# Kernel optimization log

Hardware: AMD Instinct MI355X
Metric: run time of the kernel (lower is better)

## Reference

```python
import jax, jax.numpy as jnp
import numpy as np

N, D, E, OUT = 10000, 15, 320, 30
H_INOUT = 5  # n_heads for in/out attention layers


def mha(q, k, v, wqkv, bqkv, wo, bo, nheads):
    # q,k,v: [B, L, E]; torch.nn.MultiheadAttention math (unbatched per node)
    B, L, Ed = q.shape
    hd = Ed // nheads
    wq, wk, wv = jnp.split(wqkv, 3, axis=0)
    bq, bk, bv = jnp.split(bqkv, 3)
    q2 = (q @ wq.T + bq).reshape(B, L, nheads, hd)
    k2 = (k @ wk.T + bk).reshape(B, -1, nheads, hd)
    v2 = (v @ wv.T + bv).reshape(B, -1, nheads, hd)
    scores = jnp.einsum('blhd,bmhd->bhlm', q2, k2) * (hd ** -0.5)
    a = jax.nn.softmax(scores, axis=-1)
    o = jnp.einsum('bhlm,bmhd->blhd', a, v2).reshape(B, L, Ed)
    return o @ wo.T + bo


def attn_layer(seq, Wq, Wk, Wv, wqkv, bqkv, wo, bo, nheads):
    # AttentionLayer: custom Q/K/V projections then MultiheadAttention
    return mha(seq @ Wq, seq @ Wk, seq @ Wv, wqkv, bqkv, wo, bo, nheads)


def setup_inputs() -> dict:
    key = jax.random.key(0)
    ks = jax.random.split(key, 24)
    s = 0.05  # scale params small for numerically stable softmax
    inp = {
        'X': jax.random.normal(ks[0], (N, E), jnp.float32),
        'in_idx': jax.random.randint(ks[1], (N, D), 0, N),
        'out_idx': jax.random.randint(ks[2], (N, D), 0, N),
        'in_Wq': jax.random.uniform(ks[3], (E, E)) * s,
        'in_Wk': jax.random.uniform(ks[4], (E, E)) * s,
        'in_Wv': jax.random.uniform(ks[5], (E, E)) * s,
        'in_qkv_w': jax.random.normal(ks[6], (3 * E, E)) * s,
        'in_qkv_b': jax.random.normal(ks[7], (3 * E,)) * s,
        'in_o_w': jax.random.normal(ks[8], (E, E)) * s,
        'in_o_b': jax.random.normal(ks[9], (E,)) * s,
        'out_Wq': jax.random.uniform(ks[10], (E, E)) * s,
        'out_Wk': jax.random.uniform(ks[11], (E, E)) * s,
        'out_Wv': jax.random.uniform(ks[12], (E, E)) * s,
        'out_qkv_w': jax.random.normal(ks[13], (3 * E, E)) * s,
        'out_qkv_b': jax.random.normal(ks[14], (3 * E,)) * s,
        'out_o_w': jax.random.normal(ks[15], (E, E)) * s,
        'out_o_b': jax.random.normal(ks[16], (E,)) * s,
        'fin_qkv_w': jax.random.normal(ks[17], (3 * E, E)) * s,
        'fin_qkv_b': jax.random.normal(ks[18], (3 * E,)) * s,
        'fin_o_w': jax.random.normal(ks[19], (E, E)) * s,
        'fin_o_b': jax.random.normal(ks[20], (E,)) * s,
        'W': jax.random.uniform(ks[21], (E, OUT)) * s,
    }
    return inp


def reference(X, in_idx, out_idx, in_Wq, in_Wk, in_Wv, in_qkv_w, in_qkv_b,
              in_o_w, in_o_b, out_Wq, out_Wk, out_Wv, out_qkv_w, out_qkv_b,
              out_o_w, out_o_b, fin_qkv_w, fin_qkv_b, fin_o_w, fin_o_b, W):
    # per-node sequence: [self ; neighbors] -> [N, D+1, E]
    seq_in = jnp.concatenate([X[:, None, :], X[in_idx]], axis=1)
    seq_out = jnp.concatenate([X[:, None, :], X[out_idx]], axis=1)
    a_in = attn_layer(seq_in, in_Wq, in_Wk, in_Wv, in_qkv_w, in_qkv_b,
                      in_o_w, in_o_b, H_INOUT)
    a_out = attn_layer(seq_out, out_Wq, out_Wk, out_Wv, out_qkv_w, out_qkv_b,
                       out_o_w, out_o_b, H_INOUT)
    att = jnp.concatenate([a_in, a_out], axis=1)  # [N, 2(D+1), E]
    fin = mha(att, att, att, fin_qkv_w, fin_qkv_b, fin_o_w, fin_o_b, 1)
    # first token of final attention per node -> project -> ELU
    return jax.nn.elu(fin[:, 0, :] @ W)
```

## Files before the change

kernel.cpp:

```cpp
#include <hip/hip_runtime.h>
#include <hip/hip_bf16.h>

typedef __hip_bfloat16 bf16;
typedef __bf16 nbf;
typedef nbf bf16x8 __attribute__((ext_vector_type(8)));
typedef float f32x4 __attribute__((ext_vector_type(4)));

#define NNODE 10000
#define DDEG  15
#define EE    320
#define LL    16
#define NH    5
#define HD    64
#define OUTD  30
#define PCOLS 1920
#define KF    642
#define TSTB  648

__global__ void detect_dtype_kernel(const unsigned int* __restrict__ X, int* __restrict__ flag)
{
    __shared__ int cnt;
    if (threadIdx.x == 0) cnt = 0;
    __syncthreads();
    int local = 0;
    for (int i = threadIdx.x; i < 1024; i += 256) {
        unsigned int lo = X[i] & 0xFFFFu;
        int e = (int)((lo >> 7) & 0xFFu);
        if (e >= 100 && e <= 140) local++;
    }
    atomicAdd(&cnt, local);
    __syncthreads();
    if (threadIdx.x == 0) *flag = (cnt > 512) ? 1 : 0;
}

__global__ void convert_bf_kernel(const void* __restrict__ src, nbf* __restrict__ dst,
                                  int n, const int* __restrict__ flag)
{
    int i = blockIdx.x * 256 + threadIdx.x;
    if (i >= n) return;
    if (*flag) dst[i] = ((const nbf*)src)[i];
    else       dst[i] = (nbf)(((const float*)src)[i]);
}

#define NSEG 18
struct ConvTab {
    const void* src[NSEG];
    void*       dst[NSEG];
    int         n[NSEG];
    int         tobf[NSEG];
};

__global__ void convert_batch_kernel(ConvTab t, const int* __restrict__ flag)
{
    const int seg = blockIdx.y;
    const int i = blockIdx.x * 256 + threadIdx.x;
    if (i >= t.n[seg]) return;
    float v = (*flag) ? (float)(((const nbf*)t.src[seg])[i]) : ((const float*)t.src[seg])[i];
    if (t.tobf[seg]) ((nbf*)t.dst[seg])[i] = (nbf)v;
    else             ((float*)t.dst[seg])[i] = v;
}

__global__ __launch_bounds__(256) void transpose3_kernel(const void* s0, const void* s1,
        const void* s2, nbf* __restrict__ dstbase, const int* __restrict__ flag)
{
    const void* src = (blockIdx.z == 0) ? s0 : (blockIdx.z == 1) ? s1 : s2;
    nbf* dst = dstbase + (size_t)blockIdx.z * EE * EE;
    __shared__ nbf tile[32][33];
    const int bx = blockIdx.x * 32, by = blockIdx.y * 32;
    const int tx = threadIdx.x & 31, ty = threadIdx.x >> 5;
    const int f = *flag;
    #pragma unroll
    for (int i = 0; i < 4; ++i) {
        const int r = by + ty + i * 8;
        float v = f ? (float)(((const nbf*)src)[(long)r * EE + bx + tx])
                    : ((const float*)src)[(long)r * EE + bx + tx];
        tile[ty + i * 8][tx] = (nbf)v;
    }
    __syncthreads();
    #pragma unroll
    for (int i = 0; i < 4; ++i) {
        const int r = bx + ty + i * 8;
        dst[(long)r * EE + by + tx] = tile[tx][ty + i * 8];
    }
}

__device__ __forceinline__ void stor(float* p, float v) { *p = v; }
__device__ __forceinline__ void stor(bf16* p, float v) { *p = __float2bfloat16(v); }

template<bool AT, bool BT, typename OT>
__global__ __launch_bounds__(256) void gemm_k(const float* __restrict__ A, int lda,
                       const float* __restrict__ B, int ldb,
                       const float* __restrict__ bias,
                       OT* __restrict__ C, int ldc, int M, int Nn, int K)
{
    __shared__ float As[16][65];
    __shared__ float Bs[16][65];
    const int tid = threadIdx.x;
    const int tx = tid & 15, ty = tid >> 4;
    const int n0 = blockIdx.x * 64, m0 = blockIdx.y * 64;
    float acc[4][4] = {};
    for (int k0 = 0; k0 < K; k0 += 16) {
        if constexpr (AT) {
            for (int i = tid; i < 1024; i += 256) {
                int kk = i >> 6, r = i & 63;
                int gm = m0 + r, gk = k0 + kk;
                As[kk][r] = (gm < M && gk < K) ? A[(long)gk * lda + gm] : 0.f;
            }
        } else {
            for (int i = tid; i < 1024; i += 256) {
                int r = i >> 4, kk = i & 15;
                int gm = m0 + r, gk = k0 + kk;
                As[kk][r] = (gm < M && gk < K) ? A[(long)gm * lda + gk] : 0.f;
            }
        }
        if constexpr (BT) {
            for (int i = tid; i < 1024; i += 256) {
                int r = i >> 4, kk = i & 15;
                int gn = n0 + r, gk = k0 + kk;
                Bs[kk][r] = (gn < Nn && gk < K) ? B[(long)gn * ldb + gk] : 0.f;
            }
        } else {
            for (int i = tid; i < 1024; i += 256) {
                int kk = i >> 6, c = i & 63;
                int gk = k0 + kk, gn = n0 + c;
                Bs[kk][c] = (gk < K && gn < Nn) ? B[(long)gk * ldb + gn] : 0.f;
            }
        }
        __syncthreads();
        #pragma unroll
        for (int kk = 0; kk < 16; ++kk) {
            float ra[4], rb[4];
            #pragma unroll
            for (int a = 0; a < 4; ++a) ra[a] = As[kk][ty * 4 + a];
            #pragma unroll
            for (int b = 0; b < 4; ++b) rb[b] = Bs[kk][tx * 4 + b];
            #pragma unroll
            for (int a = 0; a < 4; ++a)
                #pragma unroll
                for (int b = 0; b < 4; ++b)
                    acc[a][b] += ra[a] * rb[b];
        }
        __syncthreads();
    }
    #pragma unroll
    for (int a = 0; a < 4; ++a) {
        int gm = m0 + ty * 4 + a;
        if (gm >= M) continue;
        #pragma unroll
        for (int b = 0; b < 4; ++b) {
            int gn = n0 + tx * 4 + b;
            if (gn >= Nn) continue;
            float v = acc[a][b] + (bias ? bias[gn] : 0.f);
            stor(&C[(long)gm * ldc + gn], v);
        }
    }
}

template<typename OT>
__global__ __launch_bounds__(256) void gemm_mfma(const nbf* __restrict__ A, int lda,
        const nbf* __restrict__ Bt, int ldb, const float* __restrict__ bias,
        OT* __restrict__ C, int ldc, int M, int Nn, int K)
{
    __shared__ __align__(16) nbf As[128][40];
    __shared__ __align__(16) nbf Bs[128][40];
    const int tid = threadIdx.x;
    const int lane = tid & 63, wave = tid >> 6;
    const int wr = (wave >> 1) * 64, wc = (wave & 1) * 64;
    const int m0 = blockIdx.y * 128, n0 = blockIdx.x * 128;
    const int lr = lane & 15, lq = lane >> 4;
    f32x4 acc[4][4];
    #pragma unroll
    for (int i = 0; i < 4; ++i)
        #pragma unroll
        for (int j = 0; j < 4; ++j) { acc[i][j][0]=0.f; acc[i][j][1]=0.f; acc[i][j][2]=0.f; acc[i][j][3]=0.f; }

    for (int k0 = 0; k0 < K; k0 += 32) {
        #pragma unroll
        for (int v = tid; v < 512; v += 256) {
            const int row = v >> 2, cv = (v & 3) << 3;
            const int gk = k0 + cv;
            {
                const int gm = m0 + row;
                bf16x8 val;
                if (gm < M && gk + 8 <= K) {
                    val = *(const bf16x8*)(A + (long)gm * lda + gk);
                } else {
                    union { bf16x8 v8; nbf e[8]; } u;
                    #pragma unroll
                    for (int j = 0; j < 8; ++j) {
                        float x = (gm < M && gk + j < K) ? (float)A[(long)gm * lda + gk + j] : 0.f;
                        u.e[j] = (nbf)x;
                    }
                    val = u.v8;
                }
                *(bf16x8*)&As[row][cv] = val;
            }
            {
                const int gn = n0 + row;
                bf16x8 val;
                if (gn < Nn && gk + 8 <= K) {
                    val = *(const bf16x8*)(Bt + (long)gn * ldb + gk);
                } else {
                    union { bf16x8 v8; nbf e[8]; } u;
                    #pragma unroll
                    for (int j = 0; j < 8; ++j) {
                        float x = (gn < Nn && gk + j < K) ? (float)Bt[(long)gn * ldb + gk + j] : 0.f;
                        u.e[j] = (nbf)x;
                    }
                    val = u.v8;
                }
                *(bf16x8*)&Bs[row][cv] = val;
            }
        }
        __syncthreads();
        bf16x8 af[4], bfv[4];
        #pragma unroll
        for (int i = 0; i < 4; ++i) af[i] = *(const bf16x8*)&As[wr + i * 16 + lr][lq * 8];
        #pragma unroll
        for (int j = 0; j < 4; ++j) bfv[j] = *(const bf16x8*)&Bs[wc + j * 16 + lr][lq * 8];
        #pragma unroll
        for (int i = 0; i < 4; ++i)
            #pragma unroll
            for (int j = 0; j < 4; ++j)
                acc[i][j] = __builtin_amdgcn_mfma_f32_16x16x32_bf16(af[i], bfv[j], acc[i][j], 0, 0, 0);
        __syncthreads();
    }
    #pragma unroll
    for (int i = 0; i < 4; ++i) {
        #pragma unroll
        for (int j = 0; j < 4; ++j) {
            const int gn = n0 + wc + j * 16 + lr;
            if (gn >= Nn) continue;
            const float bv = bias ? bias[gn] : 0.f;
            #pragma unroll
            for (int r = 0; r < 4; ++r) {
                const int gm = m0 + wr + i * 16 + lq * 4 + r;
                if (gm < M) stor(&C[(long)gm * ldc + gn], acc[i][j][r] + bv);
            }
        }
    }
}

#define NJOB 11
struct JobTab {
    const nbf* A[NJOB];
    const nbf* B[NJOB];
    nbf*       C[NJOB];
};

__global__ __launch_bounds__(256) void gemm_mfma_jobs(JobTab jt)
{
    const nbf* A  = jt.A[blockIdx.z];
    const nbf* Bt = jt.B[blockIdx.z];
    nbf* C        = jt.C[blockIdx.z];
    __shared__ __align__(16) nbf As[128][40];
    __shared__ __align__(16) nbf Bs[128][40];
    const int tid = threadIdx.x;
    const int lane = tid & 63, wave = tid >> 6;
    const int wr = (wave >> 1) * 64, wc = (wave & 1) * 64;
    const int m0 = blockIdx.y * 128, n0 = blockIdx.x * 128;
    const int lr = lane & 15, lq = lane >> 4;
    f32x4 acc[4][4];
    #pragma unroll
    for (int i = 0; i < 4; ++i)
        #pragma unroll
        for (int j = 0; j < 4; ++j) { acc[i][j][0]=0.f; acc[i][j][1]=0.f; acc[i][j][2]=0.f; acc[i][j][3]=0.f; }
    for (int k0 = 0; k0 < EE; k0 += 32) {
        #pragma unroll
        for (int v = tid; v < 512; v += 256) {
            const int row = v >> 2, cv = (v & 3) << 3;
            const int gk = k0 + cv;
            const int gm = m0 + row, gn = n0 + row;
            bf16x8 va = {}, vb = {};
            if (gm < EE) va = *(const bf16x8*)(A + (long)gm * EE + gk);
            if (gn < EE) vb = *(const bf16x8*)(Bt + (long)gn * EE + gk);
            *(bf16x8*)&As[row][cv] = va;
            *(bf16x8*)&Bs[row][cv] = vb;
        }
        __syncthreads();
        bf16x8 af[4], bfv[4];
        #pragma unroll
        for (int i = 0; i < 4; ++i) af[i] = *(const bf16x8*)&As[wr + i * 16 + lr][lq * 8];
        #pragma unroll
        for (int j = 0; j < 4; ++j) bfv[j] = *(const bf16x8*)&Bs[wc + j * 16 + lr][lq * 8];
        #pragma unroll
        for (int i = 0; i < 4; ++i)
            #pragma unroll
            for (int j = 0; j < 4; ++j)
                acc[i][j] = __builtin_amdgcn_mfma_f32_16x16x32_bf16(af[i], bfv[j], acc[i][j], 0, 0, 0);
        __syncthreads();
    }
    #pragma unroll
    for (int i = 0; i < 4; ++i)
        #pragma unroll
        for (int j = 0; j < 4; ++j) {
            const int gn = n0 + wc + j * 16 + lr;
            if (gn >= EE) continue;
            #pragma unroll
            for (int r = 0; r < 4; ++r) {
                const int gm = m0 + wr + i * 16 + lq * 4 + r;
                if (gm < EE) C[(long)gm * EE + gn] = (nbf)acc[i][j][r];
            }
        }
}

__global__ __launch_bounds__(320) void compose_bias_kernel(
        const float* __restrict__ in_o_b, const float* __restrict__ out_o_b,
        const float* __restrict__ fin_qkv_w, const float* __restrict__ fin_qkv_b,
        float* __restrict__ bqc_in, nbf* __restrict__ Kcat, nbf* __restrict__ VcatN)
{
    const int which = blockIdx.x;
    const int b = threadIdx.x;
    const float* ob = (which == 2 || which == 4) ? out_o_b : in_o_b;
    const int off = (which == 0) ? 0 : (which <= 2) ? 320 : 640;
    float acc = fin_qkv_b[off + b];
    const float* wr = fin_qkv_w + (long)(off + b) * EE;
    for (int e = 0; e < EE; ++e) acc += ob[e] * wr[e];
    if (which == 0)      bqc_in[b] = acc;
    else if (which == 1) Kcat[(long)640 * EE + b] = (nbf)acc;
    else if (which == 2) Kcat[(long)641 * EE + b] = (nbf)acc;
    else if (which == 3) VcatN[(long)640 * EE + b] = (nbf)acc;
    else                 VcatN[(long)641 * EE + b] = (nbf)acc;
}

__global__ void compose_bfin(const float* __restrict__ fin_o_b, const float* __restrict__ W,
                             float* __restrict__ bfin)
{
    int j = threadIdx.x;
    if (j >= OUTD) return;
    float acc = 0.f;
    for (int e = 0; e < EE; ++e) acc += fin_o_b[e] * W[e * OUTD + j];
    bfin[j] = acc;
}

__global__ void compose_bT(const float* __restrict__ bqc, const nbf* __restrict__ Kcat,
                           float* __restrict__ bT)
{
    int c = blockIdx.x * 256 + threadIdx.x;
    if (c >= KF) return;
    const nbf* kr = Kcat + (long)c * EE;
    float acc = 0.f;
    for (int b = 0; b < EE; ++b) acc += bqc[b] * (float)kr[b];
    bT[c] = acc;
}

__global__ void ut_prep_kernel(const float* __restrict__ WWT, nbf* __restrict__ Ut)
{
    int v = blockIdx.x * 256 + threadIdx.x;
    if (v >= 64 * EE) return;
    int n = v / EE, e = v % EE;
    float val = 0.f;
    if (n < OUTD) val = WWT[(long)n * KF + e];
    else if (n >= 32 && n < 32 + OUTD) val = WWT[(long)(n - 32) * KF + 320 + e];
    Ut[v] = (nbf)val;
}

__global__ __launch_bounds__(256) void row0_kernel(const nbf* __restrict__ P,
        const int* __restrict__ in_idx, nbf* __restrict__ Orow0)
{
    const int tid = threadIdx.x, lane = tid & 63, wave = tid >> 6;
    const int node = blockIdx.x * 4 + wave;
    __shared__ float a_sh[4][16];
    __shared__ int srcs_sh[4][16];
    const int m = lane & 15, q4 = lane >> 4;
    const int src = (m == 0) ? node : in_idx[node * DDEG + m - 1];
    if (q4 == 0) srcs_sh[wave][m] = src;
    const nbf* qrow = P + (long)node * PCOLS;
    const nbf* krow = P + (long)src * PCOLS + 320;
    #pragma unroll
    for (int h = 0; h < NH; ++h) {
        float s = 0.f;
        bf16x8 q1 = *(const bf16x8*)(qrow + h * 64 + q4 * 16);
        bf16x8 q2 = *(const bf16x8*)(qrow + h * 64 + q4 * 16 + 8);
        bf16x8 k1 = *(const bf16x8*)(krow + h * 64 + q4 * 16);
        bf16x8 k2 = *(const bf16x8*)(krow + h * 64 + q4 * 16 + 8);
        #pragma unroll
        for (int j = 0; j < 8; ++j)
            s += (float)q1[j] * (float)k1[j] + (float)q2[j] * (float)k2[j];
        s += __shfl_xor(s, 16);
        s += __shfl_xor(s, 32);
        s *= 0.125f;
        float mxv = s;
        #pragma unroll
        for (int msk = 8; msk >= 1; msk >>= 1) mxv = fmaxf(mxv, __shfl_xor(mxv, msk));
        float e = __expf(s - mxv);
        float es = e;
        #pragma unroll
        for (int msk = 8; msk >= 1; msk >>= 1) es += __shfl_xor(es, msk);
        if (q4 == 0) a_sh[wave][m] = e / es;
        float o = 0.f;
        #pragma unroll
        for (int mm = 0; mm < 16; ++mm)
            o += a_sh[wave][mm] * (float)P[(long)srcs_sh[wave][mm] * PCOLS + 640 + h * 64 + lane];
        Orow0[(long)node * EE + h * 64 + lane] = (nbf)o;
    }
}

__global__ __launch_bounds__(320) void attn_y_kernel(const nbf* __restrict__ P,
        const int* __restrict__ in_idx, const int* __restrict__ out_idx,
        const nbf* __restrict__ Tb, const nbf* __restrict__ Ut,
        float* __restrict__ Ygl, int node_base)
{
    const int bx = blockIdx.x;
    const int lnode = bx >> 1, d = bx & 1;
    const int node = node_base + lnode;
    const int tid = threadIdx.x;
    const int lane = tid & 63, wave = tid >> 6;
    __shared__ __align__(16) nbf v_s[16][328];
    __shared__ __align__(16) nbf p_s[NH][16][16];
    __shared__ float Yp[NH][16][32];
    const int* idx = d ? out_idx : in_idx;
    const long coloff = (long)d * 960;
    const int lr = lane & 15, lq = lane >> 4;
    #pragma unroll
    for (int v = tid; v < 640; v += 320) {
        const int row = v / 40, c8 = (v % 40) * 8;
        const int src = (row == 0) ? node : idx[node * DDEG + row - 1];
        *(bf16x8*)&v_s[row][c8] = *(const bf16x8*)(P + (long)src * PCOLS + coloff + 640 + c8);
    }
    const int msrc = (lr == 0) ? node : idx[node * DDEG + lr - 1];
    const nbf* prow = P + (long)msrc * PCOLS + coloff;
    f32x4 sc = {0.f, 0.f, 0.f, 0.f};
    #pragma unroll
    for (int c = 0; c < 2; ++c) {
        bf16x8 aq = *(const bf16x8*)(prow + wave * 64 + c * 32 + lq * 8);
        bf16x8 bk = *(const bf16x8*)(prow + 320 + wave * 64 + c * 32 + lq * 8);
        sc = __builtin_amdgcn_mfma_f32_16x16x32_bf16(aq, bk, sc, 0, 0, 0);
    }
    float pr[4], mx4[4], sm4[4];
    #pragma unroll
    for (int r = 0; r < 4; ++r) { pr[r] = sc[r] * 0.125f; mx4[r] = pr[r]; }
    #pragma unroll
    for (int msk = 8; msk >= 1; msk >>= 1)
        #pragma unroll
        for (int r = 0; r < 4; ++r) mx4[r] = fmaxf(mx4[r], __shfl_xor(mx4[r], msk));
    #pragma unroll
    for (int r = 0; r < 4; ++r) { pr[r] = __expf(pr[r] - mx4[r]); sm4[r] = pr[r]; }
    #pragma unroll
    for (int msk = 8; msk >= 1; msk >>= 1)
        #pragma unroll
        for (int r = 0; r < 4; ++r) sm4[r] += __shfl_xor(sm4[r], msk);
    #pragma unroll
    for (int r = 0; r < 4; ++r) p_s[wave][lq * 4 + r][lr] = (nbf)(pr[r] / sm4[r]);
    union { bf16x8 v8; nbf e[8]; } pf;
    #pragma unroll
    for (int j = 0; j < 8; ++j) pf.e[j] = (nbf)0.f;
    if (lq < 2) pf.v8 = *(const bf16x8*)&p_s[wave][lr][lq * 8];
    __syncthreads();
    #pragma unroll
    for (int t = 0; t < 4; ++t) {
        const int e0 = wave * 64 + t * 16;
        union { bf16x8 v8; nbf e[8]; } af;
        #pragma unroll
        for (int j = 0; j < 8; ++j) af.e[j] = (nbf)0.f;
        if (lq < 2) {
            #pragma unroll
            for (int j = 0; j < 8; ++j) af.e[j] = v_s[lq * 8 + j][e0 + lr];
        }
        f32x4 ov = {0.f, 0.f, 0.f, 0.f};
        ov = __builtin_amdgcn_mfma_f32_16x16x32_bf16(af.v8, pf.v8, ov, 0, 0, 0);
        union { unsigned long long u; nbf e[4]; } o4;
        #pragma unroll
        for (int r = 0; r < 4; ++r) o4.e[r] = (nbf)ov[r];
        *(unsigned long long*)&v_s[lr][e0 + lq * 4] = o4.u;
    }
    const nbf* Utd = Ut + (long)d * 32 * EE;
    const nbf* TbRow = Tb + (long)node * TSTB + (long)d * 320;
    f32x4 yacc[2];
    yacc[0][0]=0.f; yacc[0][1]=0.f; yacc[0][2]=0.f; yacc[0][3]=0.f;
    yacc[1][0]=0.f; yacc[1][1]=0.f; yacc[1][2]=0.f; yacc[1][3]=0.f;
    const int e0w = wave * 64;
    #pragma unroll
    for (int c = 0; c < 2; ++c) {
        const int kk = e0w + c * 32 + lq * 8;
        bf16x8 afy = *(const bf16x8*)&v_s[lr][kk];
        #pragma unroll
        for (int nt = 0; nt < 2; ++nt) {
            const int row = nt * 16 + lr;
            const nbf* bp = (row == 31) ? (TbRow + kk) : (Utd + (long)row * EE + kk);
            bf16x8 bfy = *(const bf16x8*)bp;
            yacc[nt] = __builtin_amdgcn_mfma_f32_16x16x32_bf16(afy, bfy, yacc[nt], 0, 0, 0);
        }
    }
    #pragma unroll
    for (int nt = 0; nt < 2; ++nt)
        #pragma unroll
        for (int r = 0; r < 4; ++r)
            Yp[wave][lq * 4 + r][nt * 16 + lr] = yacc[nt][r];
    __syncthreads();
    float* yout = Ygl + (long)(lnode * 2 + d) * 512;
    for (int v = tid; v < 512; v += 320) {
        float sme = 0.f;
        #pragma unroll
        for (int w = 0; w < NH; ++w) sme += Yp[w][v >> 5][v & 31];
        yout[v] = sme;
    }
}

__global__ __launch_bounds__(256) void combine_kernel(const float* __restrict__ Ygl,
        const nbf* __restrict__ Tb, const float* __restrict__ WWT,
        const float* __restrict__ bfin, void* __restrict__ out,
        long obase, int cnt, const int* __restrict__ flag)
{
    const int tid = threadIdx.x, lane = tid & 63, wave = tid >> 6;
    const int node = blockIdx.x * 4 + wave;
    const int nodec = (node < cnt) ? node : (cnt - 1);
    __shared__ float Yl[4][1024];
    __shared__ float sf[4][32];
    const float* ysrc = Ygl + (long)nodec * 1024;
    #pragma unroll
    for (int v = lane; v < 1024; v += 64) Yl[wave][v] = ysrc[v];
    if (lane < 32) {
        const int d = lane >> 4, m = lane & 15;
        sf[wave][lane] = (Yl[wave][d * 512 + m * 32 + 31]
                          + (float)Tb[(long)nodec * TSTB + 640 + d]) * 0.05590169943749474f;
    }
    float mx = -1e30f;
    #pragma unroll 4
    for (int m = 0; m < 32; ++m) mx = fmaxf(mx, sf[wave][m]);
    float esum = 0.f, a_in = 0.f, a_out = 0.f;
    #pragma unroll 4
    for (int m = 0; m < 32; ++m) {
        float e = __expf(sf[wave][m] - mx);
        esum += e;
        if (m < 16) a_in += e; else a_out += e;
    }
    const float inv = 1.f / esum;
    a_in *= inv; a_out *= inv;
    const int j = lane;
    if (j < OUTD && node < cnt) {
        float acc = 0.f;
        #pragma unroll 4
        for (int dm = 0; dm < 32; ++dm) {
            const int d = dm >> 4, m = dm & 15;
            float a = __expf(sf[wave][dm] - mx) * inv;
            acc += a * Yl[wave][d * 512 + m * 32 + j];
        }
        float r = acc + a_in * WWT[(long)j * KF + 640]
                + a_out * WWT[(long)j * KF + 641] + bfin[j];
        r = r > 0.f ? r : expm1f(r);
        if (*flag) ((bf16*)out)[obase + (long)node * OUTD + j] = __float2bfloat16(r);
        else       ((float*)out)[obase + (long)node * OUTD + j] = r;
    }
}

extern "C" void kernel_launch(void* const* d_in, const int* in_sizes, int n_in,
                              void* d_out, int out_size, void* d_ws, size_t ws_size,
                              hipStream_t stream)
{
    const int* in_idx  = (const int*)d_in[1];
    const int* out_idx = (const int*)d_in[2];

    char* p = (char*)d_ws;
    auto alloc = [&](size_t bytes) { char* r = p; p += (bytes + 255) & ~(size_t)255; return r; };
    const size_t EE2 = (size_t)EE * EE;
    int*   flag       = (int*)alloc(256);
    nbf*   X_bf       = (nbf*)alloc((size_t)NNODE * EE * 2);
    nbf*   qkvw6_bf   = (nbf*)alloc(6 * EE2 * 2);
    nbf*   Wg6_bf     = (nbf*)alloc(6 * EE2 * 2);
    nbf*   qkvw_fin_bf= (nbf*)alloc(3 * EE2 * 2);
    nbf*   owT        = (nbf*)alloc(3 * EE2 * 2);
    float* qkvw_fin_f = (float*)alloc(3 * EE2 * 4);
    float* qkvb_fin_f = (float*)alloc(3 * EE * 4);
    float* bcat       = (float*)alloc(PCOLS * 4);
    float* ob_in_f    = (float*)alloc(EE * 4);
    float* ob_out_f   = (float*)alloc(EE * 4);
    float* ob_fin_f   = (float*)alloc(EE * 4);
    float* W_f        = (float*)alloc((size_t)EE * OUTD * 4);
    float* ow_fin_f   = (float*)alloc(EE2 * 4);
    nbf*   AcatT  = (nbf*)alloc((size_t)PCOLS * EE * 2);
    nbf*   Qc_bf  = (nbf*)alloc(EE2 * 2);
    nbf*   Kcat   = (nbf*)alloc((size_t)KF * EE * 2);
    float* bqc_in = (float*)alloc(EE * 4);
    nbf*   M2T    = (nbf*)alloc((size_t)KF * EE * 2);
    float* bT     = (float*)alloc(KF * 4);
    nbf*   VcatN  = (nbf*)alloc((size_t)KF * EE * 2);
    nbf*   WfinT  = (nbf*)alloc((size_t)OUTD * EE * 2);
    float* WWT    = (float*)alloc((size_t)OUTD * KF * 4);
    float* bfin   = (float*)alloc(64 * 4);
    nbf*   Ut     = (nbf*)alloc((size_t)64 * EE * 2);
    nbf*   P      = (nbf*)alloc((size_t)NNODE * PCOLS * 2);
    nbf*   Orow0  = (nbf*)alloc((size_t)NNODE * EE * 2);
    nbf*   Tb     = (nbf*)alloc((size_t)NNODE * TSTB * 2);
    size_t fixed = (size_t)(p - (char*)d_ws);

    const size_t per_node = 1024 * 4;
    size_t avail = (ws_size > fixed + 65536) ? (ws_size - fixed - 65536) : 0;
    long chunk_l = (long)(avail / per_node);
    chunk_l = (chunk_l / 4) * 4;
    int chunk = (chunk_l > NNODE) ? NNODE : (chunk_l < 4 ? 4 : (int)chunk_l);
    float* Ygl = (float*)alloc((size_t)chunk * 1024 * 4);

    dim3 blk(256);
    detect_dtype_kernel<<<1, blk, 0, stream>>>((const unsigned int*)d_in[0], flag);
    convert_bf_kernel<<<(NNODE * EE + 255) / 256, blk, 0, stream>>>(d_in[0], X_bf, NNODE * EE, flag);
    ConvTab ct;
    int s = 0;
    auto seg = [&](const void* src, void* dst, int n, int tobf) {
        ct.src[s] = src; ct.dst[s] = dst; ct.n[s] = n; ct.tobf[s] = tobf; ++s;
    };
    seg(d_in[6],  qkvw6_bf,           (int)(3 * EE2), 1);
    seg(d_in[13], qkvw6_bf + 3 * EE2, (int)(3 * EE2), 1);
    seg(d_in[3],  Wg6_bf + 0 * EE2, (int)EE2, 1);
    seg(d_in[4],  Wg6_bf + 1 * EE2, (int)EE2, 1);
    seg(d_in[5],  Wg6_bf + 2 * EE2, (int)EE2, 1);
    seg(d_in[10], Wg6_bf + 3 * EE2, (int)EE2, 1);
    seg(d_in[11], Wg6_bf + 4 * EE2, (int)EE2, 1);
    seg(d_in[12], Wg6_bf + 5 * EE2, (int)EE2, 1);
    seg(d_in[17], qkvw_fin_bf, (int)(3 * EE2), 1);
    seg(d_in[17], qkvw_fin_f,  (int)(3 * EE2), 0);
    seg(d_in[18], qkvb_fin_f, 3 * EE, 0);
    seg(d_in[7],  bcat,       3 * EE, 0);
    seg(d_in[14], bcat + 960, 3 * EE, 0);
    seg(d_in[9],  ob_in_f,  EE, 0);
    seg(d_in[16], ob_out_f, EE, 0);
    seg(d_in[20], ob_fin_f, EE, 0);
    seg(d_in[21], W_f, EE * OUTD, 0);
    seg(d_in[19], ow_fin_f, (int)EE2, 0);
    convert_batch_kernel<<<dim3((3 * (int)EE2 + 255) / 256, NSEG), blk, 0, stream>>>(ct, flag);
    transpose3_kernel<<<dim3(10, 10, 3), blk, 0, stream>>>(d_in[8], d_in[15], d_in[19], owT, flag);

    JobTab jt;
    for (int g = 0; g < 6; ++g) {
        jt.A[g] = qkvw6_bf + (size_t)g * EE2;
        jt.B[g] = Wg6_bf + (size_t)g * EE2;
        jt.C[g] = AcatT + (size_t)g * EE2;
    }
    jt.A[6] = owT;             jt.B[6] = qkvw_fin_bf;                      jt.C[6] = Qc_bf;
    jt.A[7] = owT;             jt.B[7] = qkvw_fin_bf + (size_t)320 * EE;   jt.C[7] = Kcat;
    jt.A[8] = owT + EE2;       jt.B[8] = qkvw_fin_bf + (size_t)320 * EE;   jt.C[8] = Kcat + (size_t)320 * EE;
    jt.A[9] = owT;             jt.B[9] = qkvw_fin_bf + (size_t)640 * EE;   jt.C[9] = VcatN;
    jt.A[10]= owT + EE2;       jt.B[10]= qkvw_fin_bf + (size_t)640 * EE;   jt.C[10]= VcatN + (size_t)320 * EE;
    gemm_mfma_jobs<<<dim3(3, 3, NJOB), blk, 0, stream>>>(jt);
    compose_bias_kernel<<<5, 320, 0, stream>>>(ob_in_f, ob_out_f, qkvw_fin_f, qkvb_fin_f,
                                               bqc_in, Kcat, VcatN);
    gemm_mfma<bf16><<<dim3(3, 6), blk, 0, stream>>>(
        Kcat, EE, Qc_bf, EE, nullptr, (bf16*)M2T, EE, KF, EE, EE);
    compose_bT<<<3, blk, 0, stream>>>(bqc_in, Kcat, bT);
    gemm_k<true, false, bf16><<<dim3(5, 1), blk, 0, stream>>>(
        W_f, OUTD, ow_fin_f, EE, nullptr, (bf16*)WfinT, EE, OUTD, EE, EE);
    gemm_mfma<float><<<dim3(6, 1), blk, 0, stream>>>(
        WfinT, EE, VcatN, EE, nullptr, WWT, KF, OUTD, KF, EE);
    compose_bfin<<<1, 64, 0, stream>>>(ob_fin_f, W_f, bfin);
    ut_prep_kernel<<<(64 * EE + 255) / 256, blk, 0, stream>>>(WWT, Ut);

    gemm_mfma<bf16><<<dim3(PCOLS / 128, (NNODE + 127) / 128), blk, 0, stream>>>(
        X_bf, EE, AcatT, EE, bcat, (bf16*)P, PCOLS, NNODE, PCOLS, EE);

    row0_kernel<<<NNODE / 4, blk, 0, stream>>>(P, in_idx, Orow0);

    gemm_mfma<bf16><<<dim3((KF + 127) / 128, (NNODE + 127) / 128), blk, 0, stream>>>(
        Orow0, EE, M2T, EE, bT, (bf16*)Tb, TSTB, NNODE, KF, EE);

    for (int base = 0; base < NNODE; base += chunk) {
        int cnt = (NNODE - base < chunk) ? (NNODE - base) : chunk;
        attn_y_kernel<<<2 * cnt, dim3(320), 0, stream>>>(
            P, in_idx, out_idx, Tb, Ut, Ygl, base);
        combine_kernel<<<(cnt + 3) / 4, blk, 0, stream>>>(
            Ygl, Tb + (size_t)base * TSTB, WWT, bfin, d_out, (long)base * OUTD, cnt, flag);
    }
}
```

Baseline: 497.1 us.

## Fuse attention and combine into one per-node kernel and merge small prep kernels

The two-block-per-node attention kernel and the separate combine kernel are merged into one kernel per node that loops over both directions. The per-direction partial results now stay in shared memory instead of making a round trip through a global scratch buffer, and the chunked launch loop is gone. Several tiny setup kernels are merged (bias plus bfin, bT plus Ut prep), and the GEMM gains a fast load path without bounds checks for full tiles. The cost is half as many blocks in the attention stage, each doing serialized work across both directions.

```diff
diff --git a/kernel.cpp b/kernel.cpp
--- a/kernel.cpp
+++ b/kernel.cpp
@@ -168,6 +168,7 @@
     const int wr = (wave >> 1) * 64, wc = (wave & 1) * 64;
     const int m0 = blockIdx.y * 128, n0 = blockIdx.x * 128;
     const int lr = lane & 15, lq = lane >> 4;
+    const bool full = (m0 + 128 <= M) && (n0 + 128 <= Nn);
     f32x4 acc[4][4];
     #pragma unroll
     for (int i = 0; i < 4; ++i)
@@ -175,41 +176,51 @@
         for (int j = 0; j < 4; ++j) { acc[i][j][0]=0.f; acc[i][j][1]=0.f; acc[i][j][2]=0.f; acc[i][j][3]=0.f; }
 
     for (int k0 = 0; k0 < K; k0 += 32) {
-        #pragma unroll
-        for (int v = tid; v < 512; v += 256) {
-            const int row = v >> 2, cv = (v & 3) << 3;
-            const int gk = k0 + cv;
-            {
-                const int gm = m0 + row;
-                bf16x8 val;
-                if (gm < M && gk + 8 <= K) {
-                    val = *(const bf16x8*)(A + (long)gm * lda + gk);
-                } else {
-                    union { bf16x8 v8; nbf e[8]; } u;
-                    #pragma unroll
-                    for (int j = 0; j < 8; ++j) {
-                        float x = (gm < M && gk + j < K) ? (float)A[(long)gm * lda + gk + j] : 0.f;
-                        u.e[j] = (nbf)x;
+        if (full) {
+            #pragma unroll
+            for (int v = tid; v < 512; v += 256) {
+                const int row = v >> 2, cv = (v & 3) << 3;
+                const int gk = k0 + cv;
+                *(bf16x8*)&As[row][cv] = *(const bf16x8*)(A + (long)(m0 + row) * lda + gk);
+                *(bf16x8*)&Bs[row][cv] = *(const bf16x8*)(Bt + (long)(n0 + row) * ldb + gk);
+            }
+        } else {
+            #pragma unroll
+            for (int v = tid; v < 512; v += 256) {
+                const int row = v >> 2, cv = (v & 3) << 3;
+                const int gk = k0 + cv;
+                {
+                    const int gm = m0 + row;
+                    bf16x8 val;
+                    if (gm < M && gk + 8 <= K) {
+                        val = *(const bf16x8*)(A + (long)gm * lda + gk);
+                    } else {
+                        union { bf16x8 v8; nbf e[8]; } u;
+                        #pragma unroll
+                        for (int j = 0; j < 8; ++j) {
+                            float x = (gm < M && gk + j < K) ? (float)A[(long)gm * lda + gk + j] : 0.f;
+                            u.e[j] = (nbf)x;
+                        }
+                        val = u.v8;
                     }
-                    val = u.v8;
+                    *(bf16x8*)&As[row][cv] = val;
                 }
-                *(bf16x8*)&As[row][cv] = val;
-            }
-            {
-                const int gn = n0 + row;
-                bf16x8 val;
-                if (gn < Nn && gk + 8 <= K) {
-                    val = *(const bf16x8*)(Bt + (long)gn * ldb + gk);
-                } else {
-                    union { bf16x8 v8; nbf e[8]; } u;
-                    #pragma unroll
-                    for (int j = 0; j < 8; ++j) {
-                        float x = (gn < Nn && gk + j < K) ? (float)Bt[(long)gn * ldb + gk + j] : 0.f;
-                        u.e[j] = (nbf)x;
+                {
+                    const int gn = n0 + row;
+                    bf16x8 val;
+                    if (gn < Nn && gk + 8 <= K) {
+                        val = *(const bf16x8*)(Bt + (long)gn * ldb + gk);
+                    } else {
+                        union { bf16x8 v8; nbf e[8]; } u;
+                        #pragma unroll
+                        for (int j = 0; j < 8; ++j) {
+                            float x = (gn < Nn && gk + j < K) ? (float)Bt[(long)gn * ldb + gk + j] : 0.f;
+                            u.e[j] = (nbf)x;
+                        }
+                        val = u.v8;
                     }
-                    val = u.v8;
+                    *(bf16x8*)&Bs[row][cv] = val;
                 }
-                *(bf16x8*)&Bs[row][cv] = val;
             }
         }
         __syncthreads();
@@ -304,13 +315,22 @@
         }
 }
 
-__global__ __launch_bounds__(320) void compose_bias_kernel(
+__global__ __launch_bounds__(320) void compose_bias_bfin_kernel(
         const float* __restrict__ in_o_b, const float* __restrict__ out_o_b,
         const float* __restrict__ fin_qkv_w, const float* __restrict__ fin_qkv_b,
-        float* __restrict__ bqc_in, nbf* __restrict__ Kcat, nbf* __restrict__ VcatN)
+        const float* __restrict__ fin_o_b, const float* __restrict__ W,
+        float* __restrict__ bqc_in, nbf* __restrict__ Kcat, nbf* __restrict__ VcatN,
+        float* __restrict__ bfin)
 {
     const int which = blockIdx.x;
     const int b = threadIdx.x;
+    if (which == 5) {
+        if (b >= OUTD) return;
+        float acc = 0.f;
+        for (int e = 0; e < EE; ++e) acc += fin_o_b[e] * W[e * OUTD + b];
+        bfin[b] = acc;
+        return;
+    }
     const float* ob = (which == 2 || which == 4) ? out_o_b : in_o_b;
     const int off = (which == 0) ? 0 : (which <= 2) ? 320 : 640;
     float acc = fin_qkv_b[off + b];
@@ -323,36 +343,27 @@
     else                 VcatN[(long)641 * EE + b] = (nbf)acc;
 }
 
-__global__ void compose_bfin(const float* __restrict__ fin_o_b, const float* __restrict__ W,
-                             float* __restrict__ bfin)
-{
-    int j = threadIdx.x;
-    if (j >= OUTD) return;
-    float acc = 0.f;
-    for (int e = 0; e < EE; ++e) acc += fin_o_b[e] * W[e * OUTD + j];
-    bfin[j] = acc;
-}
-
-__global__ void compose_bT(const float* __restrict__ bqc, const nbf* __restrict__ Kcat,
-                           float* __restrict__ bT)
-{
-    int c = blockIdx.x * 256 + threadIdx.x;
-    if (c >= KF) return;
-    const nbf* kr = Kcat + (long)c * EE;
-    float acc = 0.f;
-    for (int b = 0; b < EE; ++b) acc += bqc[b] * (float)kr[b];
-    bT[c] = acc;
-}
-
-__global__ void ut_prep_kernel(const float* __restrict__ WWT, nbf* __restrict__ Ut)
-{
-    int v = blockIdx.x * 256 + threadIdx.x;
-    if (v >= 64 * EE) return;
-    int n = v / EE, e = v % EE;
-    float val = 0.f;
-    if (n < OUTD) val = WWT[(long)n * KF + e];
-    else if (n >= 32 && n < 32 + OUTD) val = WWT[(long)(n - 32) * KF + 320 + e];
-    Ut[v] = (nbf)val;
+__global__ __launch_bounds__(256) void compose_bT_ut_kernel(
+        const float* __restrict__ bqc, const nbf* __restrict__ Kcat,
+        const float* __restrict__ WWT, float* __restrict__ bT, nbf* __restrict__ Ut)
+{
+    const int bz = blockIdx.x;
+    if (bz < 3) {
+        int c = bz * 256 + threadIdx.x;
+        if (c >= KF) return;
+        const nbf* kr = Kcat + (long)c * EE;
+        float acc = 0.f;
+        for (int b = 0; b < EE; ++b) acc += bqc[b] * (float)kr[b];
+        bT[c] = acc;
+    } else {
+        int v = (bz - 3) * 256 + threadIdx.x;
+        if (v >= 64 * EE) return;
+        int n = v / EE, e = v % EE;
+        float val = 0.f;
+        if (n < OUTD) val = WWT[(long)n * KF + e];
+        else if (n >= 32 && n < 32 + OUTD) val = WWT[(long)(n - 32) * KF + 320 + e];
+        Ut[v] = (nbf)val;
+    }
 }
 
 __global__ __launch_bounds__(256) void row0_kernel(const nbf* __restrict__ P,
@@ -396,151 +407,142 @@
     }
 }
 
-__global__ __launch_bounds__(320) void attn_y_kernel(const nbf* __restrict__ P,
+__global__ __launch_bounds__(320) void attn_final_kernel(const nbf* __restrict__ P,
         const int* __restrict__ in_idx, const int* __restrict__ out_idx,
         const nbf* __restrict__ Tb, const nbf* __restrict__ Ut,
-        float* __restrict__ Ygl, int node_base)
-{
-    const int bx = blockIdx.x;
-    const int lnode = bx >> 1, d = bx & 1;
-    const int node = node_base + lnode;
+        const float* __restrict__ WWT, const float* __restrict__ bfin,
+        void* __restrict__ out, const int* __restrict__ flag)
+{
+    const int node = blockIdx.x;
     const int tid = threadIdx.x;
     const int lane = tid & 63, wave = tid >> 6;
     __shared__ __align__(16) nbf v_s[16][328];
     __shared__ __align__(16) nbf p_s[NH][16][16];
     __shared__ float Yp[NH][16][32];
-    const int* idx = d ? out_idx : in_idx;
-    const long coloff = (long)d * 960;
+    __shared__ float Yred[2][16][32];
+    __shared__ float sf[32];
     const int lr = lane & 15, lq = lane >> 4;
-    #pragma unroll
-    for (int v = tid; v < 640; v += 320) {
-        const int row = v / 40, c8 = (v % 40) * 8;
-        const int src = (row == 0) ? node : idx[node * DDEG + row - 1];
-        *(bf16x8*)&v_s[row][c8] = *(const bf16x8*)(P + (long)src * PCOLS + coloff + 640 + c8);
-    }
-    const int msrc = (lr == 0) ? node : idx[node * DDEG + lr - 1];
-    const nbf* prow = P + (long)msrc * PCOLS + coloff;
-    f32x4 sc = {0.f, 0.f, 0.f, 0.f};
-    #pragma unroll
-    for (int c = 0; c < 2; ++c) {
-        bf16x8 aq = *(const bf16x8*)(prow + wave * 64 + c * 32 + lq * 8);
-        bf16x8 bk = *(const bf16x8*)(prow + 320 + wave * 64 + c * 32 + lq * 8);
-        sc = __builtin_amdgcn_mfma_f32_16x16x32_bf16(aq, bk, sc, 0, 0, 0);
-    }
-    float pr[4], mx4[4], sm4[4];
-    #pragma unroll
-    for (int r = 0; r < 4; ++r) { pr[r] = sc[r] * 0.125f; mx4[r] = pr[r]; }
-    #pragma unroll
-    for (int msk = 8; msk >= 1; msk >>= 1)
-        #pragma unroll
-        for (int r = 0; r < 4; ++r) mx4[r] = fmaxf(mx4[r], __shfl_xor(mx4[r], msk));
-    #pragma unroll
-    for (int r = 0; r < 4; ++r) { pr[r] = __expf(pr[r] - mx4[r]); sm4[r] = pr[r]; }
-    #pragma unroll
-    for (int msk = 8; msk >= 1; msk >>= 1)
-        #pragma unroll
-        for (int r = 0; r < 4; ++r) sm4[r] += __shfl_xor(sm4[r], msk);
-    #pragma unroll
-    for (int r = 0; r < 4; ++r) p_s[wave][lq * 4 + r][lr] = (nbf)(pr[r] / sm4[r]);
-    union { bf16x8 v8; nbf e[8]; } pf;
-    #pragma unroll
-    for (int j = 0; j < 8; ++j) pf.e[j] = (nbf)0.f;
-    if (lq < 2) pf.v8 = *(const bf16x8*)&p_s[wave][lr][lq * 8];
+
+    for (int d = 0; d < 2; ++d) {
+        const int* idx = d ? out_idx : in_idx;
+        const long coloff = (long)d * 960;
+        #pragma unroll
+        for (int v = tid; v < 640; v += 320) {
+            const int row = v / 40, c8 = (v % 40) * 8;
+            const int src = (row == 0) ? node : idx[node * DDEG + row - 1];
+            *(bf16x8*)&v_s[row][c8] = *(const bf16x8*)(P + (long)src * PCOLS + coloff + 640 + c8);
+        }
+        const int msrc = (lr == 0) ? node : idx[node * DDEG + lr - 1];
+        const nbf* prow = P + (long)msrc * PCOLS + coloff;
+        f32x4 sc = {0.f, 0.f, 0.f, 0.f};
+        #pragma unroll
+        for (int c = 0; c < 2; ++c) {
+            bf16x8 aq = *(const bf16x8*)(prow + wave * 64 + c * 32 + lq * 8);
+            bf16x8 bk = *(const bf16x8*)(prow + 320 + wave * 64 + c * 32 + lq * 8);
+            sc = __builtin_amdgcn_mfma_f32_16x16x32_bf16(aq, bk, sc, 0, 0, 0);
+        }
+        float pr[4], mx4[4], sm4[4];
+        #pragma unroll
+        for (int r = 0; r < 4; ++r) { pr[r] = sc[r] * 0.125f; mx4[r] = pr[r]; }
+        #pragma unroll
+        for (int msk = 8; msk >= 1; msk >>= 1)
+            #pragma unroll
+            for (int r = 0; r < 4; ++r) mx4[r] = fmaxf(mx4[r], __shfl_xor(mx4[r], msk));
+        #pragma unroll
+        for (int r = 0; r < 4; ++r) { pr[r] = __expf(pr[r] - mx4[r]); sm4[r] = pr[r]; }
+        #pragma unroll
+        for (int msk = 8; msk >= 1; msk >>= 1)
+            #pragma unroll
+            for (int r = 0; r < 4; ++r) sm4[r] += __shfl_xor(sm4[r], msk);
+        #pragma unroll
+        for (int r = 0; r < 4; ++r) p_s[wave][lq * 4 + r][lr] = (nbf)(pr[r] / sm4[r]);
+        union { bf16x8 v8; nbf e[8]; } pf;
+        #pragma unroll
+        for (int j = 0; j < 8; ++j) pf.e[j] = (nbf)0.f;
+        if (lq < 2) pf.v8 = *(const bf16x8*)&p_s[wave][lr][lq * 8];
+        __syncthreads();
+        #pragma unroll
+        for (int t = 0; t < 4; ++t) {
+            const int e0 = wave * 64 + t * 16;
+            union { bf16x8 v8; nbf e[8]; } af;
+            #pragma unroll
+            for (int j = 0; j < 8; ++j) af.e[j] = (nbf)0.f;
+            if (lq < 2) {
+                #pragma unroll
+                for (int j = 0; j < 8; ++j) af.e[j] = v_s[lq * 8 + j][e0 + lr];
+            }
+            f32x4 ov = {0.f, 0.f, 0.f, 0.f};
+            ov = __builtin_amdgcn_mfma_f32_16x16x32_bf16(af.v8, pf.v8, ov, 0, 0, 0);
+            union { unsigned long long u; nbf e[4]; } o4;
+            #pragma unroll
+            for (int r = 0; r < 4; ++r) o4.e[r] = (nbf)ov[r];
+            *(unsigned long long*)&v_s[lr][e0 + lq * 4] = o4.u;
+        }
+        const nbf* Utd = Ut + (long)d * 32 * EE;
+        const nbf* TbRow = Tb + (long)node * TSTB + (long)d * 320;
+        f32x4 yacc[2];
+        yacc[0][0]=0.f; yacc[0][1]=0.f; yacc[0][2]=0.f; yacc[0][3]=0.f;
+        yacc[1][0]=0.f; yacc[1][1]=0.f; yacc[1][2]=0.f; yacc[1][3]=0.f;
+        const int e0w = wave * 64;
+        #pragma unroll
+        for (int c = 0; c < 2; ++c) {
+            const int kk = e0w + c * 32 + lq * 8;
+            bf16x8 afy = *(const bf16x8*)&v_s[lr][kk];
+            #pragma unroll
+            for (int nt = 0; nt < 2; ++nt) {
+                const int row = nt * 16 + lr;
+                const nbf* bp = (row == 31) ? (TbRow + kk) : (Utd + (long)row * EE + kk);
+                bf16x8 bfy = *(const bf16x8*)bp;
+                yacc[nt] = __builtin_amdgcn_mfma_f32_16x16x32_bf16(afy, bfy, yacc[nt], 0, 0, 0);
+            }
+        }
+        #pragma unroll
+        for (int nt = 0; nt < 2; ++nt)
+            #pragma unroll
+            for (int r = 0; r < 4; ++r)
+                Yp[wave][lq * 4 + r][nt * 16 + lr] = yacc[nt][r];
+        __syncthreads();
+        for (int v = tid; v < 512; v += 320) {
+            float sme = 0.f;
+            #pragma unroll
+            for (int w = 0; w < NH; ++w) sme += Yp[w][v >> 5][v & 31];
+            Yred[d][v >> 5][v & 31] = sme;
+        }
+        __syncthreads();
+    }
+    if (tid < 32) {
+        const int d = tid >> 4, m = tid & 15;
+        sf[tid] = (Yred[d][m][31] + (float)Tb[(long)node * TSTB + 640 + d])
+                  * 0.05590169943749474f;
+    }
     __syncthreads();
-    #pragma unroll
-    for (int t = 0; t < 4; ++t) {
-        const int e0 = wave * 64 + t * 16;
-        union { bf16x8 v8; nbf e[8]; } af;
-        #pragma unroll
-        for (int j = 0; j < 8; ++j) af.e[j] = (nbf)0.f;
-        if (lq < 2) {
-            #pragma unroll
-            for (int j = 0; j < 8; ++j) af.e[j] = v_s[lq * 8 + j][e0 + lr];
-        }
-        f32x4 ov = {0.f, 0.f, 0.f, 0.f};
-        ov = __builtin_amdgcn_mfma_f32_16x16x32_bf16(af.v8, pf.v8, ov, 0, 0, 0);
-        union { unsigned long long u; nbf e[4]; } o4;
-        #pragma unroll
-        for (int r = 0; r < 4; ++r) o4.e[r] = (nbf)ov[r];
-        *(unsigned long long*)&v_s[lr][e0 + lq * 4] = o4.u;
-    }
-    const nbf* Utd = Ut + (long)d * 32 * EE;
-    const nbf* TbRow = Tb + (long)node * TSTB + (long)d * 320;
-    f32x4 yacc[2];
-    yacc[0][0]=0.f; yacc[0][1]=0.f; yacc[0][2]=0.f; yacc[0][3]=0.f;
-    yacc[1][0]=0.f; yacc[1][1]=0.f; yacc[1][2]=0.f; yacc[1][3]=0.f;
-    const int e0w = wave * 64;
-    #pragma unroll
-    for (int c = 0; c < 2; ++c) {
-        const int kk = e0w + c * 32 + lq * 8;
-        bf16x8 afy = *(const bf16x8*)&v_s[lr][kk];
-        #pragma unroll
-        for (int nt = 0; nt < 2; ++nt) {
-            const int row = nt * 16 + lr;
-            const nbf* bp = (row == 31) ? (TbRow + kk) : (Utd + (long)row * EE + kk);
-            bf16x8 bfy = *(const bf16x8*)bp;
-            yacc[nt] = __builtin_amdgcn_mfma_f32_16x16x32_bf16(afy, bfy, yacc[nt], 0, 0, 0);
-        }
-    }
-    #pragma unroll
-    for (int nt = 0; nt < 2; ++nt)
-        #pragma unroll
-        for (int r = 0; r < 4; ++r)
-            Yp[wave][lq * 4 + r][nt * 16 + lr] = yacc[nt][r];
-    __syncthreads();
-    float* yout = Ygl + (long)(lnode * 2 + d) * 512;
-    for (int v = tid; v < 512; v += 320) {
-        float sme = 0.f;
-        #pragma unroll
-        for (int w = 0; w < NH; ++w) sme += Yp[w][v >> 5][v & 31];
-        yout[v] = sme;
-    }
-}
-
-__global__ __launch_bounds__(256) void combine_kernel(const float* __restrict__ Ygl,
-        const nbf* __restrict__ Tb, const float* __restrict__ WWT,
-        const float* __restrict__ bfin, void* __restrict__ out,
-        long obase, int cnt, const int* __restrict__ flag)
-{
-    const int tid = threadIdx.x, lane = tid & 63, wave = tid >> 6;
-    const int node = blockIdx.x * 4 + wave;
-    const int nodec = (node < cnt) ? node : (cnt - 1);
-    __shared__ float Yl[4][1024];
-    __shared__ float sf[4][32];
-    const float* ysrc = Ygl + (long)nodec * 1024;
-    #pragma unroll
-    for (int v = lane; v < 1024; v += 64) Yl[wave][v] = ysrc[v];
-    if (lane < 32) {
-        const int d = lane >> 4, m = lane & 15;
-        sf[wave][lane] = (Yl[wave][d * 512 + m * 32 + 31]
-                          + (float)Tb[(long)nodec * TSTB + 640 + d]) * 0.05590169943749474f;
-    }
-    float mx = -1e30f;
-    #pragma unroll 4
-    for (int m = 0; m < 32; ++m) mx = fmaxf(mx, sf[wave][m]);
-    float esum = 0.f, a_in = 0.f, a_out = 0.f;
-    #pragma unroll 4
-    for (int m = 0; m < 32; ++m) {
-        float e = __expf(sf[wave][m] - mx);
-        esum += e;
-        if (m < 16) a_in += e; else a_out += e;
-    }
-    const float inv = 1.f / esum;
-    a_in *= inv; a_out *= inv;
-    const int j = lane;
-    if (j < OUTD && node < cnt) {
-        float acc = 0.f;
+    if (tid < 64) {
+        float mx = -1e30f;
         #pragma unroll 4
-        for (int dm = 0; dm < 32; ++dm) {
-            const int d = dm >> 4, m = dm & 15;
-            float a = __expf(sf[wave][dm] - mx) * inv;
-            acc += a * Yl[wave][d * 512 + m * 32 + j];
-        }
-        float r = acc + a_in * WWT[(long)j * KF + 640]
-                + a_out * WWT[(long)j * KF + 641] + bfin[j];
-        r = r > 0.f ? r : expm1f(r);
-        if (*flag) ((bf16*)out)[obase + (long)node * OUTD + j] = __float2bfloat16(r);
-        else       ((float*)out)[obase + (long)node * OUTD + j] = r;
+        for (int m = 0; m < 32; ++m) mx = fmaxf(mx, sf[m]);
+        float esum = 0.f, a_in = 0.f, a_out = 0.f;
+        #pragma unroll 4
+        for (int m = 0; m < 32; ++m) {
+            float e = __expf(sf[m] - mx);
+            esum += e;
+            if (m < 16) a_in += e; else a_out += e;
+        }
+        const float inv = 1.f / esum;
+        a_in *= inv; a_out *= inv;
+        const int j = tid;
+        if (j < OUTD) {
+            float acc = 0.f;
+            #pragma unroll 4
+            for (int dm = 0; dm < 32; ++dm) {
+                float a = __expf(sf[dm] - mx) * inv;
+                acc += a * Yred[dm >> 4][dm & 15][j];
+            }
+            float r = acc + a_in * WWT[(long)j * KF + 640]
+                    + a_out * WWT[(long)j * KF + 641] + bfin[j];
+            r = r > 0.f ? r : expm1f(r);
+            if (*flag) ((bf16*)out)[(long)node * OUTD + j] = __float2bfloat16(r);
+            else       ((float*)out)[(long)node * OUTD + j] = r;
+        }
     }
 }
 
@@ -582,14 +584,6 @@
     nbf*   P      = (nbf*)alloc((size_t)NNODE * PCOLS * 2);
     nbf*   Orow0  = (nbf*)alloc((size_t)NNODE * EE * 2);
     nbf*   Tb     = (nbf*)alloc((size_t)NNODE * TSTB * 2);
-    size_t fixed = (size_t)(p - (char*)d_ws);
-
-    const size_t per_node = 1024 * 4;
-    size_t avail = (ws_size > fixed + 65536) ? (ws_size - fixed - 65536) : 0;
-    long chunk_l = (long)(avail / per_node);
-    chunk_l = (chunk_l / 4) * 4;
-    int chunk = (chunk_l > NNODE) ? NNODE : (chunk_l < 4 ? 4 : (int)chunk_l);
-    float* Ygl = (float*)alloc((size_t)chunk * 1024 * 4);
 
     dim3 blk(256);
     detect_dtype_kernel<<<1, blk, 0, stream>>>((const unsigned int*)d_in[0], flag);
@@ -632,31 +626,26 @@
     jt.A[9] = owT;             jt.B[9] = qkvw_fin_bf + (size_t)640 * EE;   jt.C[9] = VcatN;
     jt.A[10]= owT + EE2;       jt.B[10]= qkvw_fin_bf + (size_t)640 * EE;   jt.C[10]= VcatN + (size_t)320 * EE;
     gemm_mfma_jobs<<<dim3(3, 3, NJOB), blk, 0, stream>>>(jt);
-    compose_bias_kernel<<<5, 320, 0, stream>>>(ob_in_f, ob_out_f, qkvw_fin_f, qkvb_fin_f,
-                                               bqc_in, Kcat, VcatN);
+
+    gemm_mfma<bf16><<<dim3(PCOLS / 128, (NNODE + 127) / 128), blk, 0, stream>>>(
+        X_bf, EE, AcatT, EE, bcat, (bf16*)P, PCOLS, NNODE, PCOLS, EE);
+
+    compose_bias_bfin_kernel<<<6, dim3(320), 0, stream>>>(
+        ob_in_f, ob_out_f, qkvw_fin_f, qkvb_fin_f, ob_fin_f, W_f,
+        bqc_in, Kcat, VcatN, bfin);
     gemm_mfma<bf16><<<dim3(3, 6), blk, 0, stream>>>(
         Kcat, EE, Qc_bf, EE, nullptr, (bf16*)M2T, EE, KF, EE, EE);
-    compose_bT<<<3, blk, 0, stream>>>(bqc_in, Kcat, bT);
     gemm_k<true, false, bf16><<<dim3(5, 1), blk, 0, stream>>>(
         W_f, OUTD, ow_fin_f, EE, nullptr, (bf16*)WfinT, EE, OUTD, EE, EE);
     gemm_mfma<float><<<dim3(6, 1), blk, 0, stream>>>(
         WfinT, EE, VcatN, EE, nullptr, WWT, KF, OUTD, KF, EE);
-    compose_bfin<<<1, 64, 0, stream>>>(ob_fin_f, W_f, bfin);
-    ut_prep_kernel<<<(64 * EE + 255) / 256, blk, 0, stream>>>(WWT, Ut);
-
-    gemm_mfma<bf16><<<dim3(PCOLS / 128, (NNODE + 127) / 128), blk, 0, stream>>>(
-        X_bf, EE, AcatT, EE, bcat, (bf16*)P, PCOLS, NNODE, PCOLS, EE);
+    compose_bT_ut_kernel<<<83, blk, 0, stream>>>(bqc_in, Kcat, WWT, bT, Ut);
 
     row0_kernel<<<NNODE / 4, blk, 0, stream>>>(P, in_idx, Orow0);
 
     gemm_mfma<bf16><<<dim3((KF + 127) / 128, (NNODE + 127) / 128), blk, 0, stream>>>(
         Orow0, EE, M2T, EE, bT, (bf16*)Tb, TSTB, NNODE, KF, EE);
 
-    for (int base = 0; base < NNODE; base += chunk) {
-        int cnt = (NNODE - base < chunk) ? (NNODE - base) : chunk;
-        attn_y_kernel<<<2 * cnt, dim3(320), 0, stream>>>(
-            P, in_idx, out_idx, Tb, Ut, Ygl, base);
-        combine_kernel<<<(cnt + 3) / 4, blk, 0, stream>>>(
-            Ygl, Tb + (size_t)base * TSTB, WWT, bfin, d_out, (long)base * OUTD, cnt, flag);
-    }
-}
+    attn_final_kernel<<<NNODE, dim3(320), 0, stream>>>(
+        P, in_idx, out_idx, Tb, Ut, WWT, bfin, d_out, flag);
+}
```

After: 507.3 us. 1.02x slower.
